# Performance work log

Measured on AMD Instinct MI355X. Metric: run time of the kernel, lower is better.

Reference implementation:

```python
import jax, jax.numpy as jnp
import numpy as np

EPS = 1e-5  # torch BatchNorm2d default


def _conv1x1(x, w):
    # x: [n, cin, h, w], w: [cout, cin] (1x1 conv == per-pixel matmul)
    return jnp.einsum('nchw,oc->nohw', x, w)


def _bn(x, gamma, beta, mean, var):
    # inference-mode BatchNorm2d over channel dim
    scale = gamma * jax.lax.rsqrt(var + EPS)
    shift = beta - mean * scale
    return x * scale[None, :, None, None] + shift[None, :, None, None]


def setup_inputs() -> dict:
    key = jax.random.key(0)
    ks = jax.random.split(key, 24)
    n, c, h, w = 16, 256, 64, 64
    width, planes = c // 2, c
    inp = {
        'x': jax.random.normal(ks[0], (n, c, h, w), jnp.float32),
        'w_theta': jax.random.normal(ks[1], (width, c), jnp.float32) * 0.05,
        'w_phi': jax.random.normal(ks[2], (width, c), jnp.float32) * 0.05,
        'w_g': jax.random.normal(ks[3], (width, c), jnp.float32) * 0.05,
        'w_zeta': jax.random.normal(ks[4], (planes, width), jnp.float32) * 0.05,
    }
    for i, (name, dim) in enumerate([('bn1', width), ('bn2', width), ('bn3', width), ('bn4', planes)]):
        k = 5 + 4 * i
        inp[f'{name}_gamma'] = jax.random.uniform(ks[k], (dim,), jnp.float32, 0.5, 1.5)
        inp[f'{name}_beta'] = jax.random.normal(ks[k + 1], (dim,), jnp.float32) * 0.1
        inp[f'{name}_mean'] = jax.random.normal(ks[k + 2], (dim,), jnp.float32) * 0.1
        inp[f'{name}_var'] = jax.random.uniform(ks[k + 3], (dim,), jnp.float32, 0.5, 1.5)
    return inp


def reference(x, w_theta, w_phi, w_g, w_zeta,
              bn1_gamma, bn1_beta, bn1_mean, bn1_var,
              bn2_gamma, bn2_beta, bn2_mean, bn2_var,
              bn3_gamma, bn3_beta, bn3_mean, bn3_var,
              bn4_gamma, bn4_beta, bn4_mean, bn4_var):
    n, c, h, w = x.shape
    theta = jax.nn.relu(_bn(_conv1x1(x, w_theta), bn1_gamma, bn1_beta, bn1_mean, bn1_var))
    phi = jax.nn.relu(_bn(_conv1x1(x, w_phi), bn2_gamma, bn2_beta, bn2_mean, bn2_var))
    g = jax.nn.relu(_bn(_conv1x1(x, w_g), bn3_gamma, bn3_beta, bn3_mean, bn3_var))

    width = theta.shape[1]
    hw = h * w
    theta = theta.reshape(n, width, hw)  # [n, C', S]
    phi = phi.reshape(n, width, hw)      # [n, C', S]
    g = g.reshape(n, width, hw)          # [n, C', S]

    # (theta^T @ phi) @ g^T == theta^T @ (phi @ g^T): no softmax, so associativity
    # lets us contract over pixels first -> O(S*C'^2) instead of O(S^2*C').
    kv = jnp.einsum('ncs,nds->ncd', phi, g)      # [n, C', C']
    out = jnp.einsum('ncs,ncd->nsd', theta, kv)  # [n, S, C']

    # faithful to torch: reshape (not transpose) [n, S, C'] -> [n, C', h, w]
    out = out.reshape(n, width, h, w)
    out = _bn(_conv1x1(out, w_zeta), bn4_gamma, bn4_beta, bn4_mean, bn4_var)
    return jax.nn.relu(out + x)
```

## Files before the change

kernel.cpp:

```cpp
#include <hip/hip_runtime.h>

#define BN_EPS 1e-5f

typedef unsigned short u16;
typedef __bf16 bf16x8 __attribute__((ext_vector_type(8)));
typedef float floatx4 __attribute__((ext_vector_type(4)));
typedef u16 u16x4 __attribute__((ext_vector_type(4)));
typedef u16 u16x8 __attribute__((ext_vector_type(8)));

__device__ __forceinline__ u16 f2bf(float f) {
    union { float f; unsigned int u; } v; v.f = f;
    unsigned int r = (v.u + 0x7fffu + ((v.u >> 16) & 1u)) >> 16;
    return (u16)r;
}

__device__ __forceinline__ float bf2f(u16 b) {
    union { unsigned int u; float f; } v; v.u = ((unsigned int)b) << 16;
    return v.f;
}

__device__ __forceinline__ unsigned int cvtpk(float lo, float hi) {
    unsigned int r;
    asm("v_cvt_pk_bf16_f32 %0, %1, %2" : "=v"(r) : "v"(lo), "v"(hi));
    return r;
}

__device__ __forceinline__ void gld16(const void* gsrc, void* ldst) {
    __builtin_amdgcn_global_load_lds(
        (const __attribute__((address_space(1))) unsigned int*)gsrc,
        (__attribute__((address_space(3))) unsigned int*)ldst, 16, 0, 0);
}

__device__ __forceinline__ int addsw(int seg, int s) {
    return (seg + (s & 7) + ((s >> 3) & 7)) & 7;
}

__global__ __launch_bounds__(256) void prep_kernel(
    const float* __restrict__ wt, const float* __restrict__ wp,
    const float* __restrict__ wg, const float* __restrict__ wz,
    const float* __restrict__ g1, const float* __restrict__ b1,
    const float* __restrict__ m1, const float* __restrict__ v1,
    const float* __restrict__ g2, const float* __restrict__ b2,
    const float* __restrict__ m2, const float* __restrict__ v2,
    const float* __restrict__ g3, const float* __restrict__ b3,
    const float* __restrict__ m3, const float* __restrict__ v3,
    const float* __restrict__ g4, const float* __restrict__ b4,
    const float* __restrict__ m4, const float* __restrict__ v4,
    u16* __restrict__ W1bf, float* __restrict__ shift1,
    u16* __restrict__ Wzbf, float* __restrict__ shift4)
{
    int id = blockIdx.x * 256 + threadIdx.x;
    if (id < 384 * 256) {
        int r = id >> 8, c = id & 255;
        int grp = r >> 7, ch = r & 127;
        const float* wsrc = grp == 0 ? wt : (grp == 1 ? wp : wg);
        const float* gg = grp == 0 ? g1 : (grp == 1 ? g2 : g3);
        const float* bb = grp == 0 ? b1 : (grp == 1 ? b2 : b3);
        const float* mm = grp == 0 ? m1 : (grp == 1 ? m2 : m3);
        const float* vv = grp == 0 ? v1 : (grp == 1 ? v2 : v3);
        float scale = gg[ch] * rsqrtf(vv[ch] + BN_EPS);
        W1bf[id] = f2bf(wsrc[ch * 256 + c] * scale);
        if (c == 0) shift1[r] = bb[ch] - mm[ch] * scale;
    }
    if (id < 256 * 128) {
        int o = id >> 7;
        float scale = g4[o] * rsqrtf(v4[o] + BN_EPS);
        Wzbf[id] = f2bf(wz[id] * scale);
        if ((id & 127) == 0) shift4[o] = b4[o] - m4[o] * scale;
    }
}

__global__ __launch_bounds__(512, 2) void k1_kernel(
    const float* __restrict__ x, const u16* __restrict__ W1,
    const float* __restrict__ shift1,
    u16* __restrict__ theta_sm, u16* __restrict__ partials)
{
    const int sk = blockIdx.x, n = blockIdx.y;
    const int tid = threadIdx.x;
    const int w = tid >> 6, lane = tid & 63;
    const int quad = lane >> 4, l16 = lane & 15;

    __shared__ __align__(16) u16 pool[32768];
    u16* ldsA = pool;
    u16* ldsB = pool + 24576;

    floatx4 acc[3][8];
#pragma unroll
    for (int i = 0; i < 3; ++i)
#pragma unroll
        for (int j = 0; j < 8; ++j) acc[i][j] = floatx4{0.f, 0.f, 0.f, 0.f};

    const int cp = w * 4 + quad;
    const float* xb = x + ((size_t)n * 256 + 2 * cp) * 4096 + sk * 128;
    unsigned int* ldsBdw = (unsigned int*)ldsB;

    float4 xv[2][2];

    auto loadx = [&](int kc) {
#pragma unroll
        for (int ch = 0; ch < 2; ++ch)
#pragma unroll
            for (int hb = 0; hb < 2; ++hb)
                xv[ch][hb] = *((const float4*)(xb + (size_t)(kc * 64 + ch) * 4096) + hb * 16 + l16);
    };
    auto writeB = [&]() {
#pragma unroll
        for (int hb = 0; hb < 2; ++hb)
#pragma unroll
            for (int j = 0; j < 4; ++j) {
                int s = hb * 64 + l16 * 4 + j;
                ldsBdw[s * 32 + addsw(w, s) * 4 + quad] =
                    cvtpk(((const float*)&xv[0][hb])[j], ((const float*)&xv[1][hb])[j]);
            }
    };
    auto stageA = [&](int kc) {
#pragma unroll
        for (int i = 0; i < 6; ++i) {
            int op = w * 6 + i;
            int r = op * 8 + (lane >> 3);
            int lseg = (lane & 7) ^ (r & 7);
            gld16(W1 + (size_t)r * 256 + kc * 64 + lseg * 8, ldsA + op * 512);
        }
    };

    loadx(0);
    for (int kc = 0; kc < 4; ++kc) {
        writeB();
        if (kc < 3) loadx(kc + 1);
        stageA(kc);
        __syncthreads();
#pragma unroll
        for (int kk = 0; kk < 2; ++kk) {
            bf16x8 a[3];
#pragma unroll
            for (int mt = 0; mt < 3; ++mt) {
                int r = mt * 128 + w * 16 + l16;
                int phys = (kk * 4 + quad) ^ (r & 7);
                a[mt] = *(const bf16x8*)(ldsA + r * 64 + phys * 8);
            }
#pragma unroll
            for (int ni = 0; ni < 8; ++ni) {
                int s = ni * 16 + l16;
                int phys = addsw(kk * 4 + quad, s);
                bf16x8 b = *(const bf16x8*)(ldsB + s * 64 + phys * 8);
#pragma unroll
                for (int mt = 0; mt < 3; ++mt)
                    acc[mt][ni] = __builtin_amdgcn_mfma_f32_16x16x32_bf16(
                        a[mt], b, acc[mt][ni], 0, 0, 0);
            }
        }
        __syncthreads();
    }

    const int ocq = w * 16 + quad * 4;
    {
        float sh0 = shift1[ocq + 0], sh1 = shift1[ocq + 1];
        float sh2 = shift1[ocq + 2], sh3 = shift1[ocq + 3];
#pragma unroll
        for (int ni = 0; ni < 8; ++ni) {
            int s = sk * 128 + ni * 16 + l16;
            float v0 = acc[0][ni][0] + sh0, v1 = acc[0][ni][1] + sh1;
            float v2 = acc[0][ni][2] + sh2, v3 = acc[0][ni][3] + sh3;
            v0 = v0 > 0.f ? v0 : 0.f;
            v1 = v1 > 0.f ? v1 : 0.f;
            v2 = v2 > 0.f ? v2 : 0.f;
            v3 = v3 > 0.f ? v3 : 0.f;
            uint2 pk;
            pk.x = cvtpk(v0, v1);
            pk.y = cvtpk(v2, v3);
            *(uint2*)(theta_sm + (size_t)n * 524288 + (size_t)s * 128 + ocq) = pk;
        }
    }
#pragma unroll
    for (int mt = 1; mt < 3; ++mt)
#pragma unroll
        for (int r = 0; r < 4; ++r) {
            int ch = ocq + r;
            float sh = shift1[mt * 128 + ch];
#pragma unroll
            for (int ni = 0; ni < 8; ++ni) {
                int sl = ni * 16 + l16;
                int half = sl >> 6, s6 = sl & 63;
                int phys = (s6 >> 3) ^ (ch & 7);
                float val = acc[mt][ni][r] + sh;
                val = val > 0.f ? val : 0.f;
                pool[((mt - 1) * 2 + half) * 8192 + ch * 64 + phys * 8 + (s6 & 7)] = f2bf(val);
            }
        }
    __syncthreads();

    floatx4 kv[8];
#pragma unroll
    for (int i = 0; i < 8; ++i) kv[i] = floatx4{0.f, 0.f, 0.f, 0.f};
#pragma unroll
    for (int h = 0; h < 2; ++h)
#pragma unroll
        for (int kk = 0; kk < 2; ++kk) {
            int rd = w * 16 + l16;
            int physa = (kk * 4 + quad) ^ (rd & 7);
            bf16x8 a = *(const bf16x8*)(pool + (2 + h) * 8192 + rd * 64 + physa * 8);
#pragma unroll
            for (int ci = 0; ci < 8; ++ci) {
                int rc = ci * 16 + l16;
                int physb = (kk * 4 + quad) ^ (rc & 7);
                bf16x8 b = *(const bf16x8*)(pool + h * 8192 + rc * 64 + physb * 8);
                kv[ci] = __builtin_amdgcn_mfma_f32_16x16x32_bf16(a, b, kv[ci], 0, 0, 0);
            }
        }

    u16* outp = partials + (size_t)(n * 32 + sk) * 16384;
#pragma unroll
    for (int r = 0; r < 4; ++r) {
        int d = w * 16 + quad * 4 + r;
#pragma unroll
        for (int ci = 0; ci < 8; ++ci)
            outp[d * 128 + ci * 16 + l16] = f2bf(kv[ci][r]);
    }
}

__global__ __launch_bounds__(256) void kv_reduce_kernel(
    const u16* __restrict__ partials, u16* __restrict__ kvT)
{
    int n = blockIdx.y;
    int f4 = blockIdx.x * 256 + threadIdx.x;
    float s0 = 0.f, s1 = 0.f, s2 = 0.f, s3 = 0.f;
#pragma unroll
    for (int kc = 0; kc < 32; ++kc) {
        u16x4 v = *(const u16x4*)(partials + (size_t)(n * 32 + kc) * 16384 + f4 * 4);
        s0 += bf2f(v[0]); s1 += bf2f(v[1]); s2 += bf2f(v[2]); s3 += bf2f(v[3]);
    }
    u16x4 o; o[0] = f2bf(s0); o[1] = f2bf(s1); o[2] = f2bf(s2); o[3] = f2bf(s3);
    *(u16x4*)(kvT + (size_t)n * 16384 + f4 * 4) = o;
}

__global__ __launch_bounds__(512, 2) void k34_kernel(
    const u16* __restrict__ theta_sm, const u16* __restrict__ kvT,
    const u16* __restrict__ Wz, const float* __restrict__ shift4,
    const float* __restrict__ x, float* __restrict__ out)
{
    const int st = blockIdx.x, n = blockIdx.y;
    const int tid = threadIdx.x;
    const int w = tid >> 6, lane = tid & 63;
    const int quad = lane >> 4, l16 = lane & 15;

    __shared__ __align__(16) u16 pool[32768];
    u16* Y = pool + 16384;

    const u16* tbase = theta_sm + (size_t)n * 524288 + (size_t)st * 128;
    const u16* kbase = kvT + (size_t)n * 16384;

    floatx4 acc3[8];
#pragma unroll
    for (int i = 0; i < 8; ++i) acc3[i] = floatx4{0.f, 0.f, 0.f, 0.f};

    auto stageTK = [&](u16* T, u16* K, int ch) {
#pragma unroll
        for (int i = 0; i < 2; ++i) {
            int op = w * 2 + i;
            int r = op * 8 + (lane >> 3);
            int lseg = (lane & 7) ^ (r & 7);
            gld16(tbase + (size_t)r * 4096 + ch * 64 + lseg * 8, T + op * 512);
            gld16(kbase + (size_t)r * 128 + ch * 64 + lseg * 8, K + op * 512);
        }
    };
    auto stageWz = [&](int ch) {
#pragma unroll
        for (int i = 0; i < 4; ++i) {
            int op = w * 4 + i;
            int r = op * 8 + (lane >> 3);
            int lseg = (lane & 7) ^ (r & 7);
            gld16(Wz + (size_t)r * 128 + ch * 64 + lseg * 8, pool + op * 512);
        }
    };
    auto comp3 = [&](const u16* T, const u16* K) {
#pragma unroll
        for (int kk = 0; kk < 2; ++kk) {
            int rc2 = w * 16 + l16;
            int physa = (kk * 4 + quad) ^ (rc2 & 7);
            bf16x8 a = *(const bf16x8*)(T + rc2 * 64 + physa * 8);
#pragma unroll
            for (int di = 0; di < 8; ++di) {
                int rd = di * 16 + l16;
                int physb = (kk * 4 + quad) ^ (rd & 7);
                bf16x8 b = *(const bf16x8*)(K + rd * 64 + physb * 8);
                acc3[di] = __builtin_amdgcn_mfma_f32_16x16x32_bf16(a, b, acc3[di], 0, 0, 0);
            }
        }
    };

    stageTK(pool, pool + 8192, 0);
    __syncthreads();
    stageTK(pool + 16384, pool + 24576, 1);
    comp3(pool, pool + 8192);
    __syncthreads();
    stageWz(0);
    comp3(pool + 16384, pool + 24576);
    __syncthreads();

#pragma unroll
    for (int di = 0; di < 8; ++di) {
        int j = di * 16 + l16;
#pragma unroll
        for (int r = 0; r < 4; ++r) {
            int c2 = w * 16 + quad * 4 + r;
            int half = c2 >> 6, c64 = c2 & 63;
            int phys = (c64 >> 3) ^ (j & 7);
            Y[half * 8192 + j * 64 + phys * 8 + (c64 & 7)] = f2bf(acc3[di][r]);
        }
    }
    __syncthreads();

    floatx4 acc4[2][8];
#pragma unroll
    for (int i = 0; i < 2; ++i)
#pragma unroll
        for (int j = 0; j < 8; ++j) acc4[i][j] = floatx4{0.f, 0.f, 0.f, 0.f};

    auto comp4 = [&](int ch) {
#pragma unroll
        for (int kk = 0; kk < 2; ++kk) {
            bf16x8 a[2];
#pragma unroll
            for (int mi = 0; mi < 2; ++mi) {
                int r = w * 32 + mi * 16 + l16;
                int phys = (kk * 4 + quad) ^ (r & 7);
                a[mi] = *(const bf16x8*)(pool + r * 64 + phys * 8);
            }
#pragma unroll
            for (int ni = 0; ni < 8; ++ni) {
                int s = ni * 16 + l16;
                int phys = (kk * 4 + quad) ^ (s & 7);
                bf16x8 b = *(const bf16x8*)(Y + ch * 8192 + s * 64 + phys * 8);
#pragma unroll
                for (int mi = 0; mi < 2; ++mi)
                    acc4[mi][ni] = __builtin_amdgcn_mfma_f32_16x16x32_bf16(
                        a[mi], b, acc4[mi][ni], 0, 0, 0);
            }
        }
    };

    comp4(0);
    __syncthreads();
    stageWz(1);
    __syncthreads();
    comp4(1);

#pragma unroll
    for (int mi = 0; mi < 2; ++mi)
#pragma unroll
        for (int r = 0; r < 4; ++r) {
            int o = w * 32 + mi * 16 + quad * 4 + r;
            float sh = shift4[o];
#pragma unroll
            for (int ni = 0; ni < 8; ++ni) {
                int s2 = st * 128 + ni * 16 + l16;
                size_t idx = ((size_t)n * 256 + o) * 4096 + s2;
                float val = acc4[mi][ni][r] + sh + x[idx];
                out[idx] = val > 0.f ? val : 0.f;
            }
        }
}

extern "C" void kernel_launch(void* const* d_in, const int* in_sizes, int n_in,
                              void* d_out, int out_size, void* d_ws, size_t ws_size,
                              hipStream_t stream)
{
    const float* x  = (const float*)d_in[0];
    const float* wt = (const float*)d_in[1];
    const float* wp = (const float*)d_in[2];
    const float* wg = (const float*)d_in[3];
    const float* wz = (const float*)d_in[4];
    const float* bn[16];
    for (int i = 0; i < 16; ++i) bn[i] = (const float*)d_in[5 + i];

    char* ws = (char*)d_ws;
    u16*   W1bf     = (u16*)  (ws + 0);
    float* shift1   = (float*)(ws + 196608);
    u16*   Wzbf     = (u16*)  (ws + 198144);
    float* shift4   = (float*)(ws + 263680);
    u16*   theta_sm = (u16*)  (ws + 264704);
    u16*   partials = (u16*)  (ws + 17041920);
    u16*   kvT      = (u16*)  (ws + 33819136);
    float* out = (float*)d_out;

    prep_kernel<<<384, 256, 0, stream>>>(
        wt, wp, wg, wz,
        bn[0], bn[1], bn[2], bn[3],
        bn[4], bn[5], bn[6], bn[7],
        bn[8], bn[9], bn[10], bn[11],
        bn[12], bn[13], bn[14], bn[15],
        W1bf, shift1, Wzbf, shift4);

    k1_kernel<<<dim3(32, 16), 512, 0, stream>>>(x, W1bf, shift1, theta_sm, partials);
    kv_reduce_kernel<<<dim3(16, 16), 256, 0, stream>>>(partials, kvT);
    k34_kernel<<<dim3(32, 16), 512, 0, stream>>>(theta_sm, kvT, Wzbf, shift4, x, out);
}
```

Before: 193.8 us.

## Double-buffer x tile in LDS and read W1 directly from global

Replaces the single-buffer LDS loop in k1 with a ping-pong pair of B buffers, so writing the next converted x chunk overlaps the MFMA work on the current one and one barrier per k-step is removed. The W1 weight tile is no longer staged through LDS; each wave loads its A fragments straight from global memory (likely L2-resident). This cuts LDS traffic and barriers but adds global-load latency inside the MFMA loop, and the last sync still stalls.

```diff
diff --git a/kernel.cpp b/kernel.cpp
--- a/kernel.cpp
+++ b/kernel.cpp
@@ -81,8 +81,8 @@
     const int quad = lane >> 4, l16 = lane & 15;
 
     __shared__ __align__(16) u16 pool[32768];
-    u16* ldsA = pool;
-    u16* ldsB = pool + 24576;
+    u16* B0 = pool;
+    u16* B1 = pool + 8192;
 
     floatx4 acc[3][8];
 #pragma unroll
@@ -92,7 +92,6 @@
 
     const int cp = w * 4 + quad;
     const float* xb = x + ((size_t)n * 256 + 2 * cp) * 4096 + sk * 128;
-    unsigned int* ldsBdw = (unsigned int*)ldsB;
 
     float4 xv[2][2];
 
@@ -103,54 +102,56 @@
             for (int hb = 0; hb < 2; ++hb)
                 xv[ch][hb] = *((const float4*)(xb + (size_t)(kc * 64 + ch) * 4096) + hb * 16 + l16);
     };
-    auto writeB = [&]() {
+    auto writeB = [&](u16* B) {
+        unsigned int* bd = (unsigned int*)B;
 #pragma unroll
         for (int hb = 0; hb < 2; ++hb)
 #pragma unroll
             for (int j = 0; j < 4; ++j) {
                 int s = hb * 64 + l16 * 4 + j;
-                ldsBdw[s * 32 + addsw(w, s) * 4 + quad] =
+                bd[s * 32 + addsw(w, s) * 4 + quad] =
                     cvtpk(((const float*)&xv[0][hb])[j], ((const float*)&xv[1][hb])[j]);
             }
     };
-    auto stageA = [&](int kc) {
-#pragma unroll
-        for (int i = 0; i < 6; ++i) {
-            int op = w * 6 + i;
-            int r = op * 8 + (lane >> 3);
-            int lseg = (lane & 7) ^ (r & 7);
-            gld16(W1 + (size_t)r * 256 + kc * 64 + lseg * 8, ldsA + op * 512);
-        }
-    };
-
-    loadx(0);
-    for (int kc = 0; kc < 4; ++kc) {
-        writeB();
-        if (kc < 3) loadx(kc + 1);
-        stageA(kc);
-        __syncthreads();
+    auto compute = [&](int kc, const u16* B) {
 #pragma unroll
         for (int kk = 0; kk < 2; ++kk) {
             bf16x8 a[3];
 #pragma unroll
             for (int mt = 0; mt < 3; ++mt) {
-                int r = mt * 128 + w * 16 + l16;
-                int phys = (kk * 4 + quad) ^ (r & 7);
-                a[mt] = *(const bf16x8*)(ldsA + r * 64 + phys * 8);
+                a[mt] = *(const bf16x8*)(W1 + (size_t)(mt * 128 + w * 16 + l16) * 256
+                                             + kc * 64 + (kk * 4 + quad) * 8);
             }
 #pragma unroll
             for (int ni = 0; ni < 8; ++ni) {
                 int s = ni * 16 + l16;
                 int phys = addsw(kk * 4 + quad, s);
-                bf16x8 b = *(const bf16x8*)(ldsB + s * 64 + phys * 8);
+                bf16x8 b = *(const bf16x8*)(B + s * 64 + phys * 8);
 #pragma unroll
                 for (int mt = 0; mt < 3; ++mt)
                     acc[mt][ni] = __builtin_amdgcn_mfma_f32_16x16x32_bf16(
                         a[mt], b, acc[mt][ni], 0, 0, 0);
             }
         }
-        __syncthreads();
-    }
+    };
+
+    loadx(0);
+    writeB(B0);
+    loadx(1);
+    __syncthreads();
+    writeB(B1);
+    loadx(2);
+    compute(0, B0);
+    __syncthreads();
+    writeB(B0);
+    loadx(3);
+    compute(1, B1);
+    __syncthreads();
+    writeB(B1);
+    compute(2, B0);
+    __syncthreads();
+    compute(3, B1);
+    __syncthreads();
 
     const int ocq = w * 16 + quad * 4;
     {
```

Measured after the change: 196.8 us. About the same (+1.6%).
